# Kernel tuning notes

Hardware: AMD Instinct MI355X
Metric: run time of the kernel (lower is better)

Reference implementation:

```python
import jax, jax.numpy as jnp
import numpy as np

TEMPERATURE = 0.07


def sparsemax(z):
    """Sparsemax along the last axis (Martins & Astudillo, 2016)."""
    n = z.shape[-1]
    z_sorted = -jnp.sort(-z, axis=-1)                      # descending sort
    k = jnp.arange(1, n + 1, dtype=z.dtype)
    cum = jnp.cumsum(z_sorted, axis=-1)
    support = (1.0 + k * z_sorted) > cum                   # support set indicator
    k_z = jnp.sum(support, axis=-1, keepdims=True)         # support size per row
    idx = k_z.astype(jnp.int32) - 1
    cum_kz = jnp.take_along_axis(cum, idx, axis=-1)
    tau = (cum_kz - 1.0) / k_z.astype(z.dtype)             # threshold
    return jnp.maximum(z - tau, 0.0)


def setup_inputs() -> dict:
    key = jax.random.key(0)
    k1, k2 = jax.random.split(key)
    B, V, D = 2048, 2, 128
    features = jax.random.normal(k1, (B, V, D), dtype=jnp.float32)
    attention_scores = jax.random.normal(k2, (V * B, V * B), dtype=jnp.float32)
    return {"features": features, "attention_scores": attention_scores}


def reference(features, attention_scores):
    B, V, D = features.shape
    N = V * B
    dt = features.dtype

    # default mask path (labels=None, mask=None): identity over the batch
    mask = jnp.eye(B, dtype=dt)

    # L2-normalize features along feature dim, flatten views (row-major, as torch .view)
    f = features / jnp.linalg.norm(features, axis=-1, keepdims=True)
    f = f.reshape(N, D)

    # cosine similarities / temperature, row-max subtracted (detached)
    sim = jnp.matmul(f, f.T) / TEMPERATURE                  # [N, N]
    sim = sim - jax.lax.stop_gradient(jnp.max(sim, axis=-1, keepdims=True))

    big_mask = jnp.tile(mask, (V, V))                       # mask.repeat(V, V)
    eye_n = jnp.eye(N, dtype=dt)
    positive_mask = big_mask - eye_n
    negative_mask = 1.0 - big_mask

    masked_scores = sparsemax((attention_scores * negative_mask) / TEMPERATURE)

    exp_sim = jnp.exp(sim) * (positive_mask + negative_mask - masked_scores)
    log_prob = sim - jnp.log(jnp.sum(exp_sim, axis=-1, keepdims=True))

    mean_log_prob_pos = jnp.sum(log_prob * positive_mask, axis=1) / jnp.sum(positive_mask, axis=1)
    loss = -jnp.mean(mean_log_prob_pos)                     # reduction='mean'
    return loss, masked_scores
```

## Files before the change

kernel.cpp:

```cpp
#include <hip/hip_runtime.h>
#include <math.h>

#define NN   4096
#define BD   2048
#define DF   128
#define INV_T (1.0f/0.07f)
#define SUPP_CAP 32
#define CAND_CAP 128

typedef __attribute__((ext_vector_type(8))) short short8v;
typedef __attribute__((ext_vector_type(4))) float float4v;
typedef float f4a __attribute__((ext_vector_type(4), aligned(4)));

__device__ inline unsigned short f2bf_rne(float x) {
  unsigned int u = __float_as_uint(x);
  u = (u + 0x7FFFu + ((u >> 16) & 1u)) >> 16;
  return (unsigned short)u;
}
__device__ inline float bf2f(unsigned short h) {
  return __uint_as_float(((unsigned int)h) << 16);
}

__global__ void k_prep(const float* __restrict__ feat,
                       unsigned short* __restrict__ fbf,
                       float* __restrict__ Zv) {
  int gid  = blockIdx.x * blockDim.x + threadIdx.x;
  int row  = gid >> 6;
  int lane = threadIdx.x & 63;
  const float2* src = (const float2*)(feat + (size_t)row * DF);
  float2 v = src[lane];
  float ss = v.x * v.x + v.y * v.y;
  #pragma unroll
  for (int off = 1; off < 64; off <<= 1) ss += __shfl_xor(ss, off, 64);
  float inv = rsqrtf(ss);
  ushort2 o;
  o.x = f2bf_rne(v.x * inv);
  o.y = f2bf_rne(v.y * inv);
  ((ushort2*)(fbf + (size_t)row * DF))[lane] = o;
  if (gid < NN) Zv[gid] = 0.f;
}

__global__ __launch_bounds__(256) void k_sparsemax(
    const float* __restrict__ attn,
    float* __restrict__ msOut,
    int* __restrict__ suppCnt,
    int* __restrict__ suppIdx,
    float* __restrict__ suppVal) {
  __shared__ float redM[4];
  __shared__ float cand[CAND_CAP];
  __shared__ int ccnt;
  __shared__ float tauS;
  int row  = blockIdx.x;
  int tid  = threadIdx.x;
  int lane = tid & 63, wv = tid >> 6;
  const float4* arow = (const float4*)(attn + (size_t)row * NN);
  int rb = row & (BD - 1);
  float z[16];
  #pragma unroll
  for (int u = 0; u < 4; ++u) {
    int q = u * 256 + tid;
    float4 a = arow[q];
    int j = q * 4;
    z[4*u+0] = (((j+0) & (BD-1)) == rb) ? 0.f : a.x * INV_T;
    z[4*u+1] = (((j+1) & (BD-1)) == rb) ? 0.f : a.y * INV_T;
    z[4*u+2] = (((j+2) & (BD-1)) == rb) ? 0.f : a.z * INV_T;
    z[4*u+3] = (((j+3) & (BD-1)) == rb) ? 0.f : a.w * INV_T;
  }
  float m = z[0];
  #pragma unroll
  for (int u = 1; u < 16; ++u) m = fmaxf(m, z[u]);
  #pragma unroll
  for (int off = 1; off < 64; off <<= 1) m = fmaxf(m, __shfl_xor(m, off, 64));
  if (lane == 0) redM[wv] = m;
  if (tid == 0) ccnt = 0;
  __syncthreads();
  m = fmaxf(fmaxf(redM[0], redM[1]), fmaxf(redM[2], redM[3]));

  float thresh = m - 1.0f;
  #pragma unroll
  for (int u = 0; u < 16; ++u) {
    if (z[u] > thresh) {
      int slot = atomicAdd(&ccnt, 1);
      if (slot < CAND_CAP) cand[slot] = z[u];
    }
  }
  __syncthreads();

  if (tid == 0) {
    int nc = min(ccnt, CAND_CAP);
    float tau = thresh;
    #pragma unroll 1
    for (int it = 0; it < 32; ++it) {
      float S = 0.f; float C = 0.f;
      for (int e = 0; e < nc; ++e) {
        float v = cand[e];
        if (v > tau) { S += v; C += 1.f; }
      }
      float nt = (C > 0.f) ? (S - 1.0f) / C : tau;
      if (nt == tau) break;
      tau = nt;
    }
    tauS = tau;
  }
  __syncthreads();
  float tau = tauS;
  if (tid == 0) {
    int sc = 0;
    int nc = min(ccnt, CAND_CAP);
    (void)nc;
    suppCnt[row] = 0;
  }

  float* orow = msOut + (size_t)row * NN;
  __shared__ int scnt;
  if (tid == 0) scnt = 0;
  __syncthreads();
  #pragma unroll
  for (int u = 0; u < 4; ++u) {
    int j = (u * 256 + tid) * 4;
    f4a v;
    v.x = fmaxf(z[4*u+0] - tau, 0.f);
    v.y = fmaxf(z[4*u+1] - tau, 0.f);
    v.z = fmaxf(z[4*u+2] - tau, 0.f);
    v.w = fmaxf(z[4*u+3] - tau, 0.f);
    *((f4a*)(orow + j)) = v;
    if (v.x > 0.f || v.y > 0.f || v.z > 0.f || v.w > 0.f) {
      float mv[4] = {v.x, v.y, v.z, v.w};
      #pragma unroll
      for (int t = 0; t < 4; ++t) {
        if (mv[t] > 0.f) {
          int slot = atomicAdd(&scnt, 1);
          if (slot < SUPP_CAP) {
            suppIdx[row * SUPP_CAP + slot] = j + t;
            suppVal[row * SUPP_CAP + slot] = mv[t];
          }
        }
      }
    }
  }
  __syncthreads();
  if (tid == 0) suppCnt[row] = min(scnt, SUPP_CAP);
}

__global__ __launch_bounds__(256) void k_gram(
    const unsigned short* __restrict__ fbf, float* __restrict__ Zv,
    float* __restrict__ numer) {
  int tid = threadIdx.x;
  int wave = tid >> 6, lane = tid & 63;
  int c = lane & 15, quad = lane >> 4;
  int wi = wave >> 1, wj = wave & 1;
  int i0 = blockIdx.y * 128 + wi * 64;
  int j0 = blockIdx.x * 128 + wj * 64;

  const unsigned short* aBase = fbf + (size_t)(i0 + c) * DF + quad * 8;
  const unsigned short* bBase = fbf + (size_t)(j0 + c) * DF + quad * 8;

  float4v acc[4][4];
  #pragma unroll
  for (int m = 0; m < 4; ++m)
    #pragma unroll
    for (int n = 0; n < 4; ++n) acc[m][n] = (float4v){0.f, 0.f, 0.f, 0.f};

  #pragma unroll
  for (int k0 = 0; k0 < DF; k0 += 32) {
    short8v afr[4], bfr[4];
    #pragma unroll
    for (int m = 0; m < 4; ++m)
      afr[m] = *(const short8v*)(aBase + (size_t)(m * 16) * DF + k0);
    #pragma unroll
    for (int n = 0; n < 4; ++n)
      bfr[n] = *(const short8v*)(bBase + (size_t)(n * 16) * DF + k0);
    #pragma unroll
    for (int m = 0; m < 4; ++m)
      #pragma unroll
      for (int n = 0; n < 4; ++n)
        acc[m][n] = __builtin_amdgcn_mfma_f32_16x16x32_bf16(
            afr[m], bfr[n], acc[m][n], 0, 0, 0);
  }

  #pragma unroll
  for (int m = 0; m < 4; ++m) {
    #pragma unroll
    for (int r = 0; r < 4; ++r) {
      int i = i0 + m * 16 + quad * 4 + r;
      int pos = (i + BD) & (NN - 1);
      float zsum = 0.f;
      #pragma unroll
      for (int n = 0; n < 4; ++n) {
        int j = j0 + n * 16 + c;
        float simv = acc[m][n][r] * INV_T - INV_T;
        float e = __expf(simv);
        zsum += (i == j) ? 0.f : e;
        if (j == pos) numer[i] = simv;
      }
      zsum += __shfl_xor(zsum, 1, 64);
      zsum += __shfl_xor(zsum, 2, 64);
      zsum += __shfl_xor(zsum, 4, 64);
      zsum += __shfl_xor(zsum, 8, 64);
      if (c == 0) atomicAdd(&Zv[i], zsum);
    }
  }
}

__global__ __launch_bounds__(256) void k_corr(
    const unsigned short* __restrict__ fbf,
    const int* __restrict__ suppCnt, const int* __restrict__ suppIdx,
    const float* __restrict__ suppVal, float* __restrict__ Zv) {
  int tid = threadIdx.x;
  int wave = tid >> 6, lane = tid & 63;
  int row = blockIdx.x * 4 + wave;
  int cnt = suppCnt[row];
  if (cnt == 0) return;
  ushort2 a = ((const ushort2*)(fbf + (size_t)row * DF))[lane];
  float ax = bf2f(a.x), ay = bf2f(a.y);
  float corr = 0.f;
  for (int e = 0; e < cnt; ++e) {
    int j = suppIdx[row * SUPP_CAP + e];
    float v = suppVal[row * SUPP_CAP + e];
    ushort2 g = ((const ushort2*)(fbf + (size_t)j * DF))[lane];
    float s = ax * bf2f(g.x) + ay * bf2f(g.y);
    #pragma unroll
    for (int off = 1; off < 64; off <<= 1) s += __shfl_xor(s, off, 64);
    corr += __expf(s * INV_T - INV_T) * v;
  }
  if (lane == 0) atomicAdd(&Zv[row], -corr);
}

__global__ void k_loss(const float* __restrict__ Zv,
                       const float* __restrict__ numer,
                       float* __restrict__ out) {
  float acc = 0.f;
  for (int i = threadIdx.x; i < NN; i += 256)
    acc += numer[i] - logf(Zv[i]);
  #pragma unroll
  for (int off = 1; off < 64; off <<= 1) acc += __shfl_xor(acc, off, 64);
  __shared__ float red[4];
  int wv = threadIdx.x >> 6, lane = threadIdx.x & 63;
  if (lane == 0) red[wv] = acc;
  __syncthreads();
  if (threadIdx.x == 0) {
    float t = (red[0] + red[1]) + (red[2] + red[3]);
    out[0] = -t / (float)NN;
  }
}

extern "C" void kernel_launch(void* const* d_in, const int* in_sizes, int n_in,
                              void* d_out, int out_size, void* d_ws, size_t ws_size,
                              hipStream_t stream) {
  const float* feat = (const float*)d_in[0];
  const float* attn = (const float*)d_in[1];
  float* out = (float*)d_out;
  float* msOut = out + 1;

  float* Zv       = (float*)d_ws;
  float* numer    = Zv + NN;
  int*   suppCnt  = (int*)(numer + NN);
  int*   suppIdx  = suppCnt + NN;
  float* suppVal  = (float*)(suppIdx + (size_t)NN * SUPP_CAP);
  unsigned short* fbf = (unsigned short*)(suppVal + (size_t)NN * SUPP_CAP);

  k_prep<<<dim3(1024), dim3(256), 0, stream>>>(feat, fbf, Zv);
  k_sparsemax<<<dim3(4096), dim3(256), 0, stream>>>(attn, msOut, suppCnt,
                                                    suppIdx, suppVal);
  k_gram<<<dim3(32, 32), dim3(256), 0, stream>>>(fbf, Zv, numer);
  k_corr<<<dim3(1024), dim3(256), 0, stream>>>(fbf, suppCnt, suppIdx, suppVal, Zv);
  k_loss<<<dim3(1), dim3(256), 0, stream>>>(Zv, numer, out);
}
```

Before: 160.2 us.

## Exploit Gram symmetry with triangular tiling and fuse sparsemax correction into sparsemax

The Gram kernel now launches only upper-triangular 128x128 tiles, skips lower-diagonal waves on diagonal tiles, and adds each exp term to both the row and the column sums. This roughly halves the MFMA and exp work. The separate correction kernel and its support buffers are removed: the sparsemax kernel keeps candidate indices in shared memory and computes the support dot products in place. The changes add column atomics and a serial loop that maps block index to triangle position, and they drop the SUPP_CAP truncation on the support size.

```diff
diff --git a/kernel.cpp b/kernel.cpp
--- a/kernel.cpp
+++ b/kernel.cpp
@@ -5,7 +5,6 @@
 #define BD   2048
 #define DF   128
 #define INV_T (1.0f/0.07f)
-#define SUPP_CAP 32
 #define CAND_CAP 128
 
 typedef __attribute__((ext_vector_type(8))) short short8v;
@@ -42,14 +41,15 @@
 
 __global__ __launch_bounds__(256) void k_sparsemax(
     const float* __restrict__ attn,
+    const unsigned short* __restrict__ fbf,
     float* __restrict__ msOut,
-    int* __restrict__ suppCnt,
-    int* __restrict__ suppIdx,
-    float* __restrict__ suppVal) {
+    float* __restrict__ Zv) {
   __shared__ float redM[4];
   __shared__ float cand[CAND_CAP];
+  __shared__ int   cidx[CAND_CAP];
   __shared__ int ccnt;
   __shared__ float tauS;
+  __shared__ float corrS[4];
   int row  = blockIdx.x;
   int tid  = threadIdx.x;
   int lane = tid & 63, wv = tid >> 6;
@@ -78,10 +78,16 @@
 
   float thresh = m - 1.0f;
   #pragma unroll
-  for (int u = 0; u < 16; ++u) {
-    if (z[u] > thresh) {
-      int slot = atomicAdd(&ccnt, 1);
-      if (slot < CAND_CAP) cand[slot] = z[u];
+  for (int u = 0; u < 4; ++u) {
+    #pragma unroll
+    for (int t = 0; t < 4; ++t) {
+      if (z[4*u+t] > thresh) {
+        int slot = atomicAdd(&ccnt, 1);
+        if (slot < CAND_CAP) {
+          cand[slot] = z[4*u+t];
+          cidx[slot] = (u * 256 + tid) * 4 + t;
+        }
+      }
     }
   }
   __syncthreads();
@@ -104,17 +110,8 @@
   }
   __syncthreads();
   float tau = tauS;
-  if (tid == 0) {
-    int sc = 0;
-    int nc = min(ccnt, CAND_CAP);
-    (void)nc;
-    suppCnt[row] = 0;
-  }
 
   float* orow = msOut + (size_t)row * NN;
-  __shared__ int scnt;
-  if (tid == 0) scnt = 0;
-  __syncthreads();
   #pragma unroll
   for (int u = 0; u < 4; ++u) {
     int j = (u * 256 + tid) * 4;
@@ -124,33 +121,44 @@
     v.z = fmaxf(z[4*u+2] - tau, 0.f);
     v.w = fmaxf(z[4*u+3] - tau, 0.f);
     *((f4a*)(orow + j)) = v;
-    if (v.x > 0.f || v.y > 0.f || v.z > 0.f || v.w > 0.f) {
-      float mv[4] = {v.x, v.y, v.z, v.w};
-      #pragma unroll
-      for (int t = 0; t < 4; ++t) {
-        if (mv[t] > 0.f) {
-          int slot = atomicAdd(&scnt, 1);
-          if (slot < SUPP_CAP) {
-            suppIdx[row * SUPP_CAP + slot] = j + t;
-            suppVal[row * SUPP_CAP + slot] = mv[t];
-          }
-        }
-      }
-    }
-  }
-  __syncthreads();
-  if (tid == 0) suppCnt[row] = min(scnt, SUPP_CAP);
+  }
+
+  int nc = min(ccnt, CAND_CAP);
+  ushort2 fr = ((const ushort2*)(fbf + (size_t)row * DF))[lane];
+  float fx = bf2f(fr.x), fy = bf2f(fr.y);
+  float corr = 0.f;
+  for (int e = wv; e < nc; e += 4) {
+    float msv = cand[e] - tau;
+    if (msv <= 0.f) continue;
+    int j = cidx[e];
+    ushort2 g = ((const ushort2*)(fbf + (size_t)j * DF))[lane];
+    float s = fx * bf2f(g.x) + fy * bf2f(g.y);
+    #pragma unroll
+    for (int off = 1; off < 64; off <<= 1) s += __shfl_xor(s, off, 64);
+    corr += __expf(s * INV_T - INV_T) * msv;
+  }
+  if (lane == 0) corrS[wv] = corr;
+  __syncthreads();
+  if (tid == 0) {
+    float tot = (corrS[0] + corrS[1]) + (corrS[2] + corrS[3]);
+    if (tot != 0.f) atomicAdd(&Zv[row], -tot);
+  }
 }
 
 __global__ __launch_bounds__(256) void k_gram(
     const unsigned short* __restrict__ fbf, float* __restrict__ Zv,
     float* __restrict__ numer) {
+  int t = blockIdx.x, bi = 0, L = 32;
+  while (t >= L) { t -= L; --L; ++bi; }
+  int bj = bi + t;
+
   int tid = threadIdx.x;
   int wave = tid >> 6, lane = tid & 63;
   int c = lane & 15, quad = lane >> 4;
   int wi = wave >> 1, wj = wave & 1;
-  int i0 = blockIdx.y * 128 + wi * 64;
-  int j0 = blockIdx.x * 128 + wj * 64;
+  if (bi == bj && wi > wj) return;
+  int i0 = bi * 128 + wi * 64;
+  int j0 = bj * 128 + wj * 64;
 
   const unsigned short* aBase = fbf + (size_t)(i0 + c) * DF + quad * 8;
   const unsigned short* bBase = fbf + (size_t)(j0 + c) * DF + quad * 8;
@@ -178,52 +186,36 @@
             afr[m], bfr[n], acc[m][n], 0, 0, 0);
   }
 
+  float colacc[4] = {0.f, 0.f, 0.f, 0.f};
   #pragma unroll
   for (int m = 0; m < 4; ++m) {
     #pragma unroll
     for (int r = 0; r < 4; ++r) {
       int i = i0 + m * 16 + quad * 4 + r;
-      int pos = (i + BD) & (NN - 1);
-      float zsum = 0.f;
+      float zrow = 0.f;
       #pragma unroll
       for (int n = 0; n < 4; ++n) {
         int j = j0 + n * 16 + c;
         float simv = acc[m][n][r] * INV_T - INV_T;
-        float e = __expf(simv);
-        zsum += (i == j) ? 0.f : e;
-        if (j == pos) numer[i] = simv;
+        float e = (j > i) ? __expf(simv) : 0.f;
+        zrow += e;
+        colacc[n] += e;
+        if (j - i == BD) { numer[i] = simv; numer[j] = simv; }
       }
-      zsum += __shfl_xor(zsum, 1, 64);
-      zsum += __shfl_xor(zsum, 2, 64);
-      zsum += __shfl_xor(zsum, 4, 64);
-      zsum += __shfl_xor(zsum, 8, 64);
-      if (c == 0) atomicAdd(&Zv[i], zsum);
+      zrow += __shfl_xor(zrow, 1, 64);
+      zrow += __shfl_xor(zrow, 2, 64);
+      zrow += __shfl_xor(zrow, 4, 64);
+      zrow += __shfl_xor(zrow, 8, 64);
+      if (c == 0) atomicAdd(&Zv[i], zrow);
     }
   }
-}
-
-__global__ __launch_bounds__(256) void k_corr(
-    const unsigned short* __restrict__ fbf,
-    const int* __restrict__ suppCnt, const int* __restrict__ suppIdx,
-    const float* __restrict__ suppVal, float* __restrict__ Zv) {
-  int tid = threadIdx.x;
-  int wave = tid >> 6, lane = tid & 63;
-  int row = blockIdx.x * 4 + wave;
-  int cnt = suppCnt[row];
-  if (cnt == 0) return;
-  ushort2 a = ((const ushort2*)(fbf + (size_t)row * DF))[lane];
-  float ax = bf2f(a.x), ay = bf2f(a.y);
-  float corr = 0.f;
-  for (int e = 0; e < cnt; ++e) {
-    int j = suppIdx[row * SUPP_CAP + e];
-    float v = suppVal[row * SUPP_CAP + e];
-    ushort2 g = ((const ushort2*)(fbf + (size_t)j * DF))[lane];
-    float s = ax * bf2f(g.x) + ay * bf2f(g.y);
-    #pragma unroll
-    for (int off = 1; off < 64; off <<= 1) s += __shfl_xor(s, off, 64);
-    corr += __expf(s * INV_T - INV_T) * v;
-  }
-  if (lane == 0) atomicAdd(&Zv[row], -corr);
+  #pragma unroll
+  for (int n = 0; n < 4; ++n) {
+    float v = colacc[n];
+    v += __shfl_xor(v, 16, 64);
+    v += __shfl_xor(v, 32, 64);
+    if (quad == 0) atomicAdd(&Zv[j0 + n * 16 + c], v);
+  }
 }
 
 __global__ void k_loss(const float* __restrict__ Zv,
@@ -252,17 +244,12 @@
   float* out = (float*)d_out;
   float* msOut = out + 1;
 
-  float* Zv       = (float*)d_ws;
-  float* numer    = Zv + NN;
-  int*   suppCnt  = (int*)(numer + NN);
-  int*   suppIdx  = suppCnt + NN;
-  float* suppVal  = (float*)(suppIdx + (size_t)NN * SUPP_CAP);
-  unsigned short* fbf = (unsigned short*)(suppVal + (size_t)NN * SUPP_CAP);
+  float* Zv    = (float*)d_ws;
+  float* numer = Zv + NN;
+  unsigned short* fbf = (unsigned short*)(numer + NN);
 
   k_prep<<<dim3(1024), dim3(256), 0, stream>>>(feat, fbf, Zv);
-  k_sparsemax<<<dim3(4096), dim3(256), 0, stream>>>(attn, msOut, suppCnt,
-                                                    suppIdx, suppVal);
-  k_gram<<<dim3(32, 32), dim3(256), 0, stream>>>(fbf, Zv, numer);
-  k_corr<<<dim3(1024), dim3(256), 0, stream>>>(fbf, suppCnt, suppIdx, suppVal, Zv);
+  k_sparsemax<<<dim3(4096), dim3(256), 0, stream>>>(attn, fbf, msOut, Zv);
+  k_gram<<<dim3(528), dim3(256), 0, stream>>>(fbf, Zv, numer);
   k_loss<<<dim3(1), dim3(256), 0, stream>>>(Zv, numer, out);
 }
```

Measured after the change: 149.2 us. 1.07x faster.
